# Kernel tuning notes

Hardware: AMD Instinct MI355X
Metric: run time of the kernel (lower is better)

The kernel has to match this reference:

```python
import jax, jax.numpy as jnp
import numpy as np

B, DIM, H, W = 8, 128, 128, 128
QK, MLP, HEADS, NT, GS = 128, 256, 4, 8, 128


def _ln(x, w, b):
    m = jnp.mean(x, -1, keepdims=True)
    v = jnp.mean((x - m) ** 2, -1, keepdims=True)
    return (x - m) * jax.lax.rsqrt(v + 1e-5) * w + b


def _norml2(x):
    n = jnp.sqrt(jnp.sum(x * x, -1, keepdims=True))
    return x / jnp.maximum(n, 1e-12)


def setup_inputs() -> dict:
    key = jax.random.key(0)
    ks = jax.random.split(key, 12)
    s = 0.02
    f32 = jnp.float32
    return {
        'x': jax.random.normal(ks[0], (B, DIM, H, W), f32),
        'means': jax.random.normal(ks[1], (NT, DIM), f32),
        'ln1_w': jnp.ones((DIM,), f32), 'ln1_b': jnp.zeros((DIM,), f32),
        'wq': jax.random.normal(ks[2], (QK, DIM), f32) * s,
        'wk': jax.random.normal(ks[3], (QK, DIM), f32) * s,
        'wv': jax.random.normal(ks[4], (DIM, DIM), f32) * s,
        'wproj': jax.random.normal(ks[5], (DIM, DIM), f32) * s,
        'irca_wk': jax.random.normal(ks[6], (QK, DIM), f32) * s,
        'irca_wv': jax.random.normal(ks[7], (DIM, DIM), f32) * s,
        'conv1x1_w': jax.random.normal(ks[8], (DIM, DIM), f32) * s,
        'ln2_w': jnp.ones((DIM,), f32), 'ln2_b': jnp.zeros((DIM,), f32),
        'fc1_w': jax.random.normal(ks[9], (MLP, DIM), f32) * s,
        'fc1_b': jnp.zeros((MLP,), f32),
        'dw_w': jax.random.normal(ks[10], (MLP, 1, 5, 5), f32) * s,
        'dw_b': jnp.zeros((MLP,), f32),
        'fc2_w': jax.random.normal(ks[11], (DIM, MLP), f32) * s,
        'fc2_b': jnp.zeros((DIM,), f32),
    }


def reference(x, means, ln1_w, ln1_b, wq, wk, wv, wproj, irca_wk, irca_wv,
              conv1x1_w, ln2_w, ln2_b, fc1_w, fc1_b, dw_w, dw_b, fc2_w, fc2_b):
    Bx, C, Hh, Ww = x.shape
    N = Hh * Ww
    xt = x.reshape(Bx, C, N).transpose(0, 2, 1)          # b n c
    residual = xt
    xn = _ln(xt, ln1_w, ln1_b)
    m = jax.lax.stop_gradient(means)                      # eval: means buffer, detached
    # IRCA (eval path): global K/V from cluster means
    dq, dv = QK // HEADS, C // HEADS
    kg = (m @ irca_wk.T).reshape(NT, HEADS, dq).transpose(1, 0, 2)  # h nt dq
    vg = (m @ irca_wv.T).reshape(NT, HEADS, dv).transpose(1, 0, 2)  # h nt dv
    # cluster assignment -> token reordering (no grad)
    scores = jnp.einsum('bic,jc->bij', _norml2(xn), _norml2(m))
    buckets = jnp.argmax(scores, axis=-1)
    idx = jnp.argsort(buckets, axis=-1)                   # [B,N] permutation
    # IASA
    q = xn @ wq.T
    k = xn @ wk.T
    v = xn @ wv.T
    take = lambda t: jnp.take_along_axis(t, idx[:, :, None], axis=1)
    q, k, v = take(q), take(k), take(v)
    gs = min(N, GS)
    ng = (N + gs - 1) // gs
    pad_n = ng * gs - N
    qp = jnp.concatenate([q, jnp.flip(q[:, N - pad_n:N], axis=1)], axis=1)
    qp = qp.reshape(Bx, ng, gs, HEADS, dq).transpose(0, 1, 3, 2, 4)  # b g h gs dq

    def window(t, d):
        tp = jnp.concatenate([t, jnp.flip(t[:, N - pad_n - gs:N], axis=1)], axis=1)
        blk = tp.reshape(Bx, ng + 1, gs, HEADS, d)
        win = jnp.concatenate([blk[:, :-1], blk[:, 1:]], axis=2)     # b g 2gs h d
        return win.transpose(0, 1, 3, 2, 4)

    kp = window(k, dq)
    vp = window(v, dv)
    scale = 1.0 / np.sqrt(dq)
    a1 = jax.nn.softmax(jnp.einsum('bghqd,bghkd->bghqk', qp, kp) * scale, axis=-1)
    out1 = jnp.einsum('bghqk,bghkd->bghqd', a1, vp)
    a2 = jax.nn.softmax(jnp.einsum('bghqd,hkd->bghqk', qp, kg) * scale, axis=-1)
    out2 = jnp.einsum('bghqk,hkd->bghqd', a2, vg)
    out = (out1 + out2).transpose(0, 1, 3, 2, 4).reshape(Bx, ng * gs, C)[:, :N]
    inv = jnp.argsort(idx, axis=-1)                       # scatter-back = inverse perm
    out = jnp.take_along_axis(out, inv[:, :, None], axis=1)
    out = out @ wproj.T
    yimg = out.transpose(0, 2, 1).reshape(Bx, C, Hh, Ww)
    yimg = jnp.einsum('oc,bchw->bohw', conv1x1_w, yimg)
    x2 = residual + yimg.reshape(Bx, C, N).transpose(0, 2, 1)
    # ConvFFN with PreNorm
    xm = _ln(x2, ln2_w, ln2_b)
    h1 = jax.nn.gelu(xm @ fc1_w.T + fc1_b, approximate=False)
    himg = h1.transpose(0, 2, 1).reshape(Bx, MLP, Hh, Ww)
    dwc = jax.lax.conv_general_dilated(himg, dw_w, (1, 1), 'SAME',
                                       feature_group_count=MLP,
                                       dimension_numbers=('NCHW', 'OIHW', 'NCHW'))
    dwc = jax.nn.gelu(dwc + dw_b.reshape(1, MLP, 1, 1), approximate=False)
    h1 = h1 + dwc.reshape(Bx, MLP, N).transpose(0, 2, 1)
    x3 = x2 + (h1 @ fc2_w.T + fc2_b)
    return x3.transpose(0, 2, 1).reshape(Bx, C, Hh, Ww)
```

## Files before the change

kernel.cpp:

```cpp
#include <hip/hip_runtime.h>
#include <math.h>

typedef unsigned short u16;
typedef unsigned int u32;
typedef __attribute__((ext_vector_type(8))) short bf16x8;
typedef __attribute__((ext_vector_type(4))) float f32x4;

constexpr int BB   = 8;
constexpr int DIMC = 128;
constexpr int HH   = 128;
constexpr int WW   = 128;
constexpr int NTOK = HH * WW;
constexpr int QKD  = 128;
constexpr int MLPD = 256;
constexpr int NTm  = 8;
constexpr int GSZ  = 128;
constexpr int NGRP = NTOK / GSZ;
constexpr size_t BIG = 16777216;

__device__ __forceinline__ float exp2_raw(float x) {
    return __builtin_amdgcn_exp2f(x);
}
__device__ __forceinline__ float gelu_f(float v) {
    float u = v * (0.7978845608028654f + 0.035677408136300125f * v * v);
    float e = exp2_raw(u * 2.885390081777927f);
    float th = 1.0f - 2.0f * __builtin_amdgcn_rcpf(e + 1.0f);
    return 0.5f * v * (1.0f + th);
}
__device__ __forceinline__ float b2f(u16 u) {
    return __uint_as_float(((u32)u) << 16);
}
__device__ __forceinline__ u16 f2b(float f) {
    u32 x = __float_as_uint(f);
    return (u16)((x + 0x7fffu + ((x >> 16) & 1u)) >> 16);
}
__device__ __forceinline__ float ulo(u32 u) { return __uint_as_float(u << 16); }
__device__ __forceinline__ float uhi(u32 u) { return __uint_as_float(u & 0xffff0000u); }

__global__ __launch_bounds__(128) void k_prep(const float* __restrict__ means,
        const float* __restrict__ iwk, const float* __restrict__ iwv,
        float* __restrict__ mhat, u16* __restrict__ kgbb, u16* __restrict__ vgtb) {
    __shared__ float sm[DIMC];
    __shared__ float inv_s;
    int tt = blockIdx.x;
    int t = threadIdx.x;
    sm[t] = means[tt * DIMC + t];
    __syncthreads();
    if (t == 0) {
        float s = 0.f;
        for (int c = 0; c < DIMC; c++) s += sm[c] * sm[c];
        inv_s = 1.f / fmaxf(sqrtf(s), 1e-12f);
    }
    __syncthreads();
    mhat[tt * DIMC + t] = sm[t] * inv_s;
    float sk = 0.f, sv = 0.f;
    #pragma unroll 8
    for (int c = 0; c < DIMC; c++) {
        sk = fmaf(sm[c], iwk[t * DIMC + c], sk);
        sv = fmaf(sm[c], iwv[t * DIMC + c], sv);
    }
    kgbb[tt * DIMC + t] = f2b(sk);
    vgtb[(t >> 5) * 256 + (t & 31) * 8 + tt] = f2b(sv);
}

__global__ __launch_bounds__(256) void k_cvtall(const float* __restrict__ wq,
        const float* __restrict__ wk, const float* __restrict__ wv,
        const float* __restrict__ fc1, const float* __restrict__ fc2,
        u16* __restrict__ wqkv, u16* __restrict__ fc1b, u16* __restrict__ fc2b) {
    int i = blockIdx.x * 256 + threadIdx.x;
    if (i < 49152) {
        const float* s = (i < 16384) ? wq : (i < 32768 ? wk : wv);
        wqkv[i] = f2b(s[i & 16383]);
    } else if (i < 81920) {
        fc1b[i - 49152] = f2b(fc1[i - 49152]);
    } else if (i < 114688) {
        fc2b[i - 81920] = f2b(fc2[i - 81920]);
    }
}

__global__ __launch_bounds__(256) void k_fuse(const float* __restrict__ c1,
        const float* __restrict__ wp, u16* __restrict__ wf) {
    __shared__ float wpS[DIMC * DIMC];
    int t = threadIdx.x;
    for (int i = t; i < DIMC * DIMC; i += 256) wpS[i] = wp[i];
    __syncthreads();
    int o = blockIdx.x * 2 + (t >> 7);
    int c = t & 127;
    float s = 0.f;
    #pragma unroll 8
    for (int m = 0; m < DIMC; m++) s = fmaf(c1[o * DIMC + m], wpS[m * DIMC + c], s);
    wf[o * DIMC + c] = f2b(s);
}

__global__ __launch_bounds__(256) void k_ln1(const float* __restrict__ x,
        const float* __restrict__ lw, const float* __restrict__ lb,
        const float* __restrict__ mhat, u16* __restrict__ xn, int* __restrict__ bucket) {
    __shared__ float smh[NTm * DIMC];
    __shared__ float lwb[DIMC], lbb[DIMC];
    __shared__ float red[4][64][3];
    __shared__ float scr[4][64][9];
    const int chunk = blockIdx.x;
    const int b = chunk >> 8;
    const int n0 = (chunk & 255) << 6;
    const int t = threadIdx.x;
    const int cg = t >> 6, tok = t & 63;
    const int n = n0 + tok;
    const int cbase = cg * 32;
    for (int i = t; i < NTm * DIMC; i += 256) smh[i] = mhat[i];
    if (t < DIMC) { lwb[t] = lw[t]; lbb[t] = lb[t]; }

    const float* xb = x + (size_t)b * DIMC * NTOK + (size_t)cbase * NTOK + n;
    float xv[32];
    float sum = 0.f, sq = 0.f;
    #pragma unroll
    for (int c = 0; c < 32; c++) {
        float v = xb[(size_t)c * NTOK];
        xv[c] = v;
        sum += v; sq += v * v;
    }
    red[cg][tok][0] = sum;
    red[cg][tok][1] = sq;
    __syncthreads();
    float s0 = red[0][tok][0] + red[1][tok][0] + red[2][tok][0] + red[3][tok][0];
    float q0 = red[0][tok][1] + red[1][tok][1] + red[2][tok][1] + red[3][tok][1];
    float mean = s0 * (1.0f / DIMC);
    float var = q0 * (1.0f / DIMC) - mean * mean;
    float rstd = rsqrtf(var + 1e-5f);

    float sc[NTm];
    #pragma unroll
    for (int j = 0; j < NTm; j++) sc[j] = 0.f;
    u32 opk[16];
    #pragma unroll
    for (int c = 0; c < 32; c += 2) {
        float v0 = (xv[c]     - mean) * rstd * lwb[cbase + c]     + lbb[cbase + c];
        float v1 = (xv[c + 1] - mean) * rstd * lwb[cbase + c + 1] + lbb[cbase + c + 1];
        #pragma unroll
        for (int j = 0; j < NTm; j++) {
            sc[j] = fmaf(v0, smh[j * DIMC + cbase + c], sc[j]);
            sc[j] = fmaf(v1, smh[j * DIMC + cbase + c + 1], sc[j]);
        }
        opk[c >> 1] = (u32)f2b(v0) | ((u32)f2b(v1) << 16);
    }
    u16* xnr = xn + ((size_t)b * NTOK + n) * DIMC + cbase;
    *(uint4*)(xnr + 0)  = make_uint4(opk[0],  opk[1],  opk[2],  opk[3]);
    *(uint4*)(xnr + 8)  = make_uint4(opk[4],  opk[5],  opk[6],  opk[7]);
    *(uint4*)(xnr + 16) = make_uint4(opk[8],  opk[9],  opk[10], opk[11]);
    *(uint4*)(xnr + 24) = make_uint4(opk[12], opk[13], opk[14], opk[15]);

    #pragma unroll
    for (int j = 0; j < NTm; j++) scr[cg][tok][j] = sc[j];
    __syncthreads();
    if (cg == 0) {
        float v0 = ((scr[0][tok][0] + scr[1][tok][0]) + (scr[2][tok][0] + scr[3][tok][0]));
        int best = 0; float bv = v0;
        #pragma unroll
        for (int j = 1; j < NTm; j++) {
            float v = ((scr[0][tok][j] + scr[1][tok][j]) + (scr[2][tok][j] + scr[3][tok][j]));
            if (v > bv) { bv = v; best = j; }
        }
        bucket[b * NTOK + n] = best;
    }
}

__global__ __launch_bounds__(64) void k_count(const int* __restrict__ bucket, int* __restrict__ cnt) {
    int chunk = blockIdx.x;
    int bk = bucket[(chunk << 6) + threadIdx.x];
    #pragma unroll
    for (int j = 0; j < NTm; j++) {
        unsigned long long m = __ballot(bk == j);
        if (threadIdx.x == 0) cnt[chunk * NTm + j] = (int)__popcll(m);
    }
}

__global__ __launch_bounds__(64) void k_scan(const int* __restrict__ cnt, int* __restrict__ base) {
    __shared__ int sc[256 * NTm];
    __shared__ int bb[NTm], tot[NTm];
    int b = blockIdx.x, t = threadIdx.x;
    for (int i = t; i < 256 * NTm; i += 64) sc[i] = cnt[b * 256 * NTm + i];
    __syncthreads();
    if (t < NTm) {
        int run = 0;
        for (int c = 0; c < 256; c++) {
            int v = sc[c * NTm + t];
            sc[c * NTm + t] = run;
            run += v;
        }
        tot[t] = run;
    }
    __syncthreads();
    if (t == 0) {
        int a = 0;
        for (int j = 0; j < NTm; j++) { bb[j] = a; a += tot[j]; }
    }
    __syncthreads();
    for (int i = t; i < 256 * NTm; i += 64) base[b * 256 * NTm + i] = sc[i] + bb[i & 7];
}

__global__ __launch_bounds__(64) void k_place(const int* __restrict__ bucket,
        const int* __restrict__ base, int* __restrict__ gidx) {
    int chunk = blockIdx.x;
    int lane = threadIdx.x;
    int nf = (chunk << 6) + lane;
    int bk = bucket[nf];
    unsigned long long lower = (1ull << lane) - 1ull;
    int rank = 0;
    #pragma unroll
    for (int j = 0; j < NTm; j++) {
        unsigned long long m = __ballot(bk == j);
        if (bk == j) rank = (int)__popcll(m & lower);
    }
    int b = nf >> 14;
    int pos = base[chunk * NTm + bk] + rank;
    gidx[b * NTOK + pos] = nf & (NTOK - 1);
}

__global__ __launch_bounds__(256) void k_inv(const int* __restrict__ gidx, u16* __restrict__ iinv) {
    int i = blockIdx.x * 256 + threadIdx.x;
    int b = i >> 14;
    iinv[((size_t)b << 14) + gidx[i]] = (u16)(i & (NTOK - 1));
}

template<int KDIM, int NOUT, int GATHER, int AIMG, int BIASF, int GELUF, int RES, int STIMG, int CBF, int LN2F>
__global__ __launch_bounds__(256) void g_mfma(const u16* __restrict__ A, const u16* __restrict__ W,
        const float* __restrict__ bias, const void* __restrict__ resid,
        const int* __restrict__ gidx, void* __restrict__ Cout, float ascale,
        const float* __restrict__ lnw, const float* __restrict__ lnb, void* __restrict__ Cout2) {
    __shared__ u16 As[128 * 40];
    __shared__ u16 Ws[128 * 40];
    const int b = blockIdx.z;
    const int m0 = blockIdx.x * 128;
    const int n0 = blockIdx.y * 128;
    const int t = threadIdx.x;
    const int lane = t & 63;
    const int wave = t >> 6;
    const int wm = (wave & 1) * 64;
    const int wn = (wave >> 1) * 64;
    const int srow = t >> 2;
    const int sko = (t & 3) * 8;
    const u16* pA0 = nullptr; const u16* pA1 = nullptr;
    if (!AIMG) {
        int ra0 = m0 + srow, ra1 = m0 + 64 + srow;
        if (GATHER == 1) {
            ra0 = gidx[b * NTOK + ra0];
            ra1 = gidx[b * NTOK + ra1];
        } else if (GATHER == 2) {
            const u16* gi = (const u16*)gidx;
            ra0 = gi[b * NTOK + ra0];
            ra1 = gi[b * NTOK + ra1];
        }
        pA0 = A + ((size_t)b * NTOK + ra0) * KDIM + sko;
        pA1 = A + ((size_t)b * NTOK + ra1) * KDIM + sko;
    }
    const u16* pW0 = W + (size_t)(n0 + srow) * KDIM + sko;
    const u16* pW1 = W + (size_t)(n0 + 64 + srow) * KDIM + sko;

    f32x4 acc[4][4];
    #pragma unroll
    for (int i = 0; i < 4; i++)
        #pragma unroll
        for (int j = 0; j < 4; j++) acc[i][j] = (f32x4){0.f, 0.f, 0.f, 0.f};

    for (int k0 = 0; k0 < KDIM; k0 += 32) {
        uint4 a0, a1, w0, w1;
        u16 e[16];
        if (!AIMG) {
            a0 = *(const uint4*)(pA0 + k0);
            a1 = *(const uint4*)(pA1 + k0);
        } else {
            const int kk2 = t & 31;
            const int tg = t >> 5;
            const u16* src = A + ((size_t)b * KDIM + k0 + kk2) * NTOK + m0 + tg * 16;
            *(uint4*)&e[0] = *(const uint4*)src;
            *(uint4*)&e[8] = *(const uint4*)(src + 8);
        }
        w0 = *(const uint4*)(pW0 + k0);
        w1 = *(const uint4*)(pW1 + k0);
        __syncthreads();
        if (!AIMG) {
            *(uint4*)&As[srow * 40 + sko] = a0;
            *(uint4*)&As[(64 + srow) * 40 + sko] = a1;
        } else {
            const int kk2 = t & 31;
            const int tg = t >> 5;
            #pragma unroll
            for (int j = 0; j < 16; j++) As[(tg * 16 + j) * 40 + kk2] = e[j];
        }
        *(uint4*)&Ws[srow * 40 + sko] = w0;
        *(uint4*)&Ws[(64 + srow) * 40 + sko] = w1;
        __syncthreads();
        bf16x8 af[4], bfv[4];
        #pragma unroll
        for (int i = 0; i < 4; i++)
            af[i] = *(bf16x8*)&As[(wm + i * 16 + (lane & 15)) * 40 + (lane >> 4) * 8];
        #pragma unroll
        for (int j = 0; j < 4; j++)
            bfv[j] = *(bf16x8*)&Ws[(wn + j * 16 + (lane & 15)) * 40 + (lane >> 4) * 8];
        #pragma unroll
        for (int i = 0; i < 4; i++)
            #pragma unroll
            for (int j = 0; j < 4; j++)
                acc[i][j] = __builtin_amdgcn_mfma_f32_16x16x32_bf16(af[i], bfv[j], acc[i][j], 0, 0, 0);
    }

    const int c2 = lane & 15, gq2 = lane >> 4;
    int colj[4];
    #pragma unroll
    for (int j = 0; j < 4; j++) colj[j] = n0 + wn + j * 16 + c2;

    if (LN2F) {
        #pragma unroll
        for (int i = 0; i < 4; i++) {
            int rbase = m0 + wm + i * 16 + gq2 * 4;
            #pragma unroll
            for (int j = 0; j < 4; j++) {
                const float* rf = (const float*)resid;
                float4 rr = *(const float4*)&rf[((size_t)b * NOUT + colj[j]) * NTOK + rbase];
                acc[i][j][0] += rr.x; acc[i][j][1] += rr.y;
                acc[i][j][2] += rr.z; acc[i][j][3] += rr.w;
            }
        }
        __syncthreads();
        float* ps = (float*)&As[0];
        const int h = wn >> 6;
        float mean_[4][4], rstd_[4][4];
        #pragma unroll
        for (int i = 0; i < 4; i++)
            #pragma unroll
            for (int r = 0; r < 4; r++) {
                float s = 0.f, q = 0.f;
                #pragma unroll
                for (int j = 0; j < 4; j++) { float tv = acc[i][j][r]; s += tv; q += tv * tv; }
                s += __shfl_xor(s, 1, 64); q += __shfl_xor(q, 1, 64);
                s += __shfl_xor(s, 2, 64); q += __shfl_xor(q, 2, 64);
                s += __shfl_xor(s, 4, 64); q += __shfl_xor(q, 4, 64);
                s += __shfl_xor(s, 8, 64); q += __shfl_xor(q, 8, 64);
                if (c2 == 0) {
                    int rl = wm + i * 16 + gq2 * 4 + r;
                    ps[(h * 128 + rl) * 2 + 0] = s;
                    ps[(h * 128 + rl) * 2 + 1] = q;
                }
            }
        __syncthreads();
        #pragma unroll
        for (int i = 0; i < 4; i++)
            #pragma unroll
            for (int r = 0; r < 4; r++) {
                int rl = wm + i * 16 + gq2 * 4 + r;
                float s = ps[rl * 2 + 0] + ps[(128 + rl) * 2 + 0];
                float q = ps[rl * 2 + 1] + ps[(128 + rl) * 2 + 1];
                float mn = s * (1.0f / 128.0f);
                float vr = q * (1.0f / 128.0f) - mn * mn;
                mean_[i][r] = mn;
                rstd_[i][r] = rsqrtf(vr + 1e-5f);
            }
        float lwj[4], lbj[4];
        #pragma unroll
        for (int j = 0; j < 4; j++) { lwj[j] = lnw[colj[j]]; lbj[j] = lnb[colj[j]]; }
        u16* xo = (u16*)Cout;
        u16* mo = (u16*)Cout2;
        #pragma unroll
        for (int i = 0; i < 4; i++) {
            int rbase = m0 + wm + i * 16 + gq2 * 4;
            #pragma unroll
            for (int j = 0; j < 4; j++)
                #pragma unroll
                for (int r = 0; r < 4; r++) {
                    float tv = acc[i][j][r];
                    size_t off = ((size_t)b * NTOK + rbase + r) * NOUT + colj[j];
                    xo[off] = f2b(tv);
                    mo[off] = f2b((tv - mean_[i][r]) * rstd_[i][r] * lwj[j] + lbj[j]);
                }
        }
        return;
    }

    const float smul = (blockIdx.y == 0) ? ascale : 1.0f;
    float bj[4];
    #pragma unroll
    for (int j = 0; j < 4; j++) bj[j] = BIASF ? bias[colj[j]] : 0.f;
    #pragma unroll
    for (int i = 0; i < 4; i++) {
        int rbase = m0 + wm + i * 16 + gq2 * 4;
        #pragma unroll
        for (int j = 0; j < 4; j++) {
            f32x4 v = acc[i][j];
            v[0] *= smul; v[1] *= smul; v[2] *= smul; v[3] *= smul;
            if (BIASF) { v[0] += bj[j]; v[1] += bj[j]; v[2] += bj[j]; v[3] += bj[j]; }
            if (GELUF) { v[0] = gelu_f(v[0]); v[1] = gelu_f(v[1]); v[2] = gelu_f(v[2]); v[3] = gelu_f(v[3]); }
            if (RES == 1) {
                const float* rf = (const float*)resid;
                float4 rr = *(const float4*)&rf[((size_t)b * NOUT + colj[j]) * NTOK + rbase];
                v[0] += rr.x; v[1] += rr.y; v[2] += rr.z; v[3] += rr.w;
            } else if (RES == 3) {
                const u16* rb = (const u16*)resid;
                #pragma unroll
                for (int r = 0; r < 4; r++)
                    v[r] += b2f(rb[((size_t)b * NTOK + rbase + r) * NOUT + colj[j]]);
            }
            if (STIMG) {
                size_t off = ((size_t)b * NOUT + colj[j]) * NTOK + rbase;
                if (CBF) {
                    ushort4 o;
                    o.x = f2b(v[0]); o.y = f2b(v[1]); o.z = f2b(v[2]); o.w = f2b(v[3]);
                    *(ushort4*)((u16*)Cout + off) = o;
                } else {
                    *(float4*)((float*)Cout + off) = make_float4(v[0], v[1], v[2], v[3]);
                }
            } else {
                if (CBF) {
                    #pragma unroll
                    for (int r = 0; r < 4; r++)
                        ((u16*)Cout)[((size_t)b * NTOK + rbase + r) * NOUT + colj[j]] = f2b(v[r]);
                } else {
                    #pragma unroll
                    for (int r = 0; r < 4; r++)
                        ((float*)Cout)[((size_t)b * NTOK + rbase + r) * NOUT + colj[j]] = v[r];
                }
            }
        }
    }
}

__global__ __launch_bounds__(256, 3) void k_attn(const u16* __restrict__ qkv,
        const u16* __restrict__ kgbb, const u16* __restrict__ vgtb,
        u16* __restrict__ outp) {
    __shared__ u16 VT[2][32][264];
    __shared__ u16 Pb[4][64][36];
    const int g = blockIdx.x, hp = blockIdx.y, b = blockIdx.z;
    const int t = threadIdx.x;
    const int wave = t >> 6, lane = t & 63;
    const int c = lane & 15, gq = lane >> 4;
    const int lh = wave & 1, head = hp * 2 + lh, qh = wave >> 1;
    const size_t brow = (size_t)b * NTOK;
    const bool lastg = (g == NGRP - 1);

    {
        int key = t;
        int pos = (!lastg || key < GSZ) ? g * GSZ + key : NTOK - 1 - (key - GSZ);
        const u16* vp = qkv + (brow + pos) * 384 + 256 + hp * 64;
        #pragma unroll
        for (int i = 0; i < 8; i++) {
            uint4 v = *(const uint4*)(vp + i * 8);
            u16 e[8];
            *(uint4*)e = v;
            #pragma unroll
            for (int j = 0; j < 8; j++) {
                int d = i * 8 + j;
                VT[d >> 5][d & 31][key] = e[j];
            }
        }
        if (t < 64) {
            int l2 = t >> 5, dv = t & 31;
            uint4 v = *(const uint4*)(vgtb + ((size_t)(hp * 2 + l2) * 32 + dv) * 8);
            *(uint4*)&VT[l2][dv][256] = v;
        }
    }

    const int q0 = g * GSZ + qh * 64;
    bf16x8 qf[4];
    #pragma unroll
    for (int nq = 0; nq < 4; nq++)
        qf[nq] = *(const bf16x8*)(qkv + (brow + q0 + nq * 16 + c) * 384 + head * 32 + gq * 8);

    const u16* kbp = qkv + brow * 384 + 128 + head * 32 + gq * 8;
    bf16x8 kfa[8][2];
    #pragma unroll
    for (int s = 0; s < 8; s++)
        #pragma unroll
        for (int mk = 0; mk < 2; mk++) {
            int kl = s * 32 + mk * 16 + c;
            int pos = (!lastg || kl < GSZ) ? g * GSZ + kl : NTOK - 1 - (kl - GSZ);
            kfa[s][mk] = *(const bf16x8*)(kbp + (size_t)pos * 384);
        }
    bf16x8 kgf = *(const bf16x8*)(kgbb + (c & 7) * 128 + head * 32 + gq * 8);

    __syncthreads();

    f32x4 acc[4][2];
    #pragma unroll
    for (int i = 0; i < 4; i++)
        #pragma unroll
        for (int j = 0; j < 2; j++) acc[i][j] = (f32x4){0.f, 0.f, 0.f, 0.f};
    float lsum[4] = {0.f, 0.f, 0.f, 0.f};

    __builtin_amdgcn_s_setprio(1);
    for (int s = 0; s < 8; s++) {
        #pragma unroll
        for (int mk = 0; mk < 2; mk++) {
            #pragma unroll
            for (int nq = 0; nq < 4; nq++) {
                f32x4 st = __builtin_amdgcn_mfma_f32_16x16x32_bf16(kfa[s][mk], qf[nq],
                        (f32x4){0.f, 0.f, 0.f, 0.f}, 0, 0, 0);
                float p0 = exp2_raw(st[0]), p1 = exp2_raw(st[1]);
                float p2 = exp2_raw(st[2]), p3 = exp2_raw(st[3]);
                lsum[nq] += (p0 + p1) + (p2 + p3);
                u32 r0, r1;
                asm("v_cvt_pk_bf16_f32 %0, %1, %2" : "=v"(r0) : "v"(p0), "v"(p1));
                asm("v_cvt_pk_bf16_f32 %0, %1, %2" : "=v"(r1) : "v"(p2), "v"(p3));
                *(uint2*)&Pb[wave][nq * 16 + c][mk * 16 + gq * 4] = make_uint2(r0, r1);
            }
        }
        __builtin_amdgcn_sched_barrier(0);
        bf16x8 pf[4], vf[2];
        #pragma unroll
        for (int mt = 0; mt < 4; mt++)
            pf[mt] = *(const bf16x8*)&Pb[wave][mt * 16 + c][gq * 8];
        #pragma unroll
        for (int nv = 0; nv < 2; nv++)
            vf[nv] = *(const bf16x8*)&VT[lh][nv * 16 + c][s * 32 + gq * 8];
        #pragma unroll
        for (int mt = 0; mt < 4; mt++)
            #pragma unroll
            for (int nv = 0; nv < 2; nv++)
                acc[mt][nv] = __builtin_amdgcn_mfma_f32_16x16x32_bf16(pf[mt], vf[nv], acc[mt][nv], 0, 0, 0);
    }

    #pragma unroll
    for (int nq = 0; nq < 4; nq++) {
        lsum[nq] += __shfl_xor(lsum[nq], 16, 64);
        lsum[nq] += __shfl_xor(lsum[nq], 32, 64);
    }

    {
        #pragma unroll
        for (int nq = 0; nq < 4; nq++) {
            f32x4 sg = __builtin_amdgcn_mfma_f32_16x16x32_bf16(kgf, qf[nq],
                    (f32x4){0.f, 0.f, 0.f, 0.f}, 0, 0, 0);
            float p0, p1, p2, p3;
            if (gq < 2) {
                p0 = exp2_raw(sg[0]); p1 = exp2_raw(sg[1]);
                p2 = exp2_raw(sg[2]); p3 = exp2_raw(sg[3]);
            } else { p0 = p1 = p2 = p3 = 0.f; }
            float lg = (p0 + p1) + (p2 + p3);
            lg += __shfl_xor(lg, 16, 64);
            lg += __shfl_xor(lg, 32, 64);
            float w = lsum[nq] / lg;
            p0 *= w; p1 *= w; p2 *= w; p3 *= w;
            u32 r0, r1;
            asm("v_cvt_pk_bf16_f32 %0, %1, %2" : "=v"(r0) : "v"(p0), "v"(p1));
            asm("v_cvt_pk_bf16_f32 %0, %1, %2" : "=v"(r1) : "v"(p2), "v"(p3));
            *(uint2*)&Pb[wave][nq * 16 + c][gq * 4] = make_uint2(r0, r1);
        }
        __builtin_amdgcn_sched_barrier(0);
        bf16x8 zf;
        #pragma unroll
        for (int z8 = 0; z8 < 8; z8++) zf[z8] = 0;
        bf16x8 pf[4], vf[2];
        #pragma unroll
        for (int mt = 0; mt < 4; mt++)
            pf[mt] = *(const bf16x8*)&Pb[wave][mt * 16 + c][gq * 8];
        #pragma unroll
        for (int nv = 0; nv < 2; nv++)
            vf[nv] = (gq == 0) ? *(const bf16x8*)&VT[lh][nv * 16 + c][256] : zf;
        #pragma unroll
        for (int mt = 0; mt < 4; mt++)
            #pragma unroll
            for (int nv = 0; nv < 2; nv++)
                acc[mt][nv] = __builtin_amdgcn_mfma_f32_16x16x32_bf16(pf[mt], vf[nv], acc[mt][nv], 0, 0, 0);
    }
    __builtin_amdgcn_s_setprio(0);

    float* lf = (float*)&Pb[wave][0][0];
    if (gq == 0) {
        #pragma unroll
        for (int nq = 0; nq < 4; nq++) lf[nq * 16 + c] = lsum[nq];
    }
    __builtin_amdgcn_sched_barrier(0);
    u16 ov[4][2][4];
    #pragma unroll
    for (int mt = 0; mt < 4; mt++) {
        float il[4];
        #pragma unroll
        for (int r = 0; r < 4; r++)
            il[r] = 1.f / lf[mt * 16 + gq * 4 + r];
        #pragma unroll
        for (int nv = 0; nv < 2; nv++)
            #pragma unroll
            for (int r = 0; r < 4; r++)
                ov[mt][nv][r] = f2b(acc[mt][nv][r] * il[r]);
    }

    __syncthreads();
    u16* st = (u16*)&VT[0][0][0];
    #pragma unroll
    for (int mt = 0; mt < 4; mt++)
        #pragma unroll
        for (int nv = 0; nv < 2; nv++)
            #pragma unroll
            for (int r = 0; r < 4; r++)
                st[(qh * 64 + mt * 16 + gq * 4 + r) * 68 + lh * 32 + nv * 16 + c] = ov[mt][nv][r];
    __syncthreads();
    {
        const int rl0 = t >> 3;
        const int seg = t & 7;
        #pragma unroll
        for (int p = 0; p < 4; p++) {
            int rl = rl0 + p * 32;
            uint4 v4 = *(const uint4*)&st[rl * 68 + seg * 8];
            *(uint4*)&outp[(brow + g * GSZ + rl) * 128 + hp * 64 + seg * 8] = v4;
        }
    }
}

__global__ __launch_bounds__(256) void k_dw(const u16* __restrict__ himg,
        const float* __restrict__ dww, const float* __restrict__ dwb, u16* __restrict__ dsum) {
    const int mc = blockIdx.y, b = blockIdx.z;
    const int t = threadIdx.x;
    const int y = blockIdx.x * 32 + (t >> 4) * 2;
    const int xb = (t & 15) * 8;
    float wgt[25];
    #pragma unroll
    for (int i = 0; i < 25; i++) wgt[i] = dww[mc * 25 + i];
    const float bsv = dwb[mc];
    const u16* src = himg + ((size_t)b * MLPD + mc) * NTOK;
    u16* dst = dsum + ((size_t)b * MLPD + mc) * NTOK;

    float w[6][12];
    #pragma unroll
    for (int r = 0; r < 6; r++) {
        int ysrc = y - 2 + r;
        bool vy = (ysrc >= 0 && ysrc < HH);
        const u16* rp = src + ysrc * WW + xb;
        uint4 aq = vy ? *(const uint4*)(rp - 8) : make_uint4(0u, 0u, 0u, 0u);
        uint4 bq = vy ? *(const uint4*)(rp)     : make_uint4(0u, 0u, 0u, 0u);
        uint4 cq = vy ? *(const uint4*)(rp + 8) : make_uint4(0u, 0u, 0u, 0u);
        w[r][0]  = ulo(aq.w); w[r][1]  = uhi(aq.w);
        w[r][2]  = ulo(bq.x); w[r][3]  = uhi(bq.x);
        w[r][4]  = ulo(bq.y); w[r][5]  = uhi(bq.y);
        w[r][6]  = ulo(bq.z); w[r][7]  = uhi(bq.z);
        w[r][8]  = ulo(bq.w); w[r][9]  = uhi(bq.w);
        w[r][10] = ulo(cq.x); w[r][11] = uhi(cq.x);
        if (xb == 0)   { w[r][0]  = 0.f; w[r][1]  = 0.f; }
        if (xb == 120) { w[r][10] = 0.f; w[r][11] = 0.f; }
    }

    float acc0[8], acc1[8];
    #pragma unroll
    for (int px = 0; px < 8; px++) { acc0[px] = 0.f; acc1[px] = 0.f; }
    #pragma unroll
    for (int dy = 0; dy < 5; dy++)
        #pragma unroll
        for (int dx = 0; dx < 5; dx++) {
            float wv = wgt[dy * 5 + dx];
            #pragma unroll
            for (int px = 0; px < 8; px++) {
                acc0[px] = fmaf(wv, w[dy][px + dx], acc0[px]);
                acc1[px] = fmaf(wv, w[dy + 1][px + dx], acc1[px]);
            }
        }

    u32 o0[4], o1[4];
    #pragma unroll
    for (int px = 0; px < 8; px += 2) {
        u16 a0 = f2b(w[2][px + 2] + gelu_f(acc0[px] + bsv));
        u16 a1 = f2b(w[2][px + 3] + gelu_f(acc0[px + 1] + bsv));
        o0[px >> 1] = (u32)a0 | ((u32)a1 << 16);
        u16 b0 = f2b(w[3][px + 2] + gelu_f(acc1[px] + bsv));
        u16 b1 = f2b(w[3][px + 3] + gelu_f(acc1[px + 1] + bsv));
        o1[px >> 1] = (u32)b0 | ((u32)b1 << 16);
    }
    *(uint4*)(dst + y * WW + xb) = *(uint4*)o0;
    *(uint4*)(dst + (y + 1) * WW + xb) = *(uint4*)o1;
}

extern "C" void kernel_launch(void* const* d_in, const int* in_sizes, int n_in,
                              void* d_out, int out_size, void* d_ws, size_t ws_size,
                              hipStream_t stream) {
    const float* x       = (const float*)d_in[0];
    const float* means   = (const float*)d_in[1];
    const float* ln1_w   = (const float*)d_in[2];
    const float* ln1_b   = (const float*)d_in[3];
    const float* wq      = (const float*)d_in[4];
    const float* wk      = (const float*)d_in[5];
    const float* wv      = (const float*)d_in[6];
    const float* wproj   = (const float*)d_in[7];
    const float* irca_wk = (const float*)d_in[8];
    const float* irca_wv = (const float*)d_in[9];
    const float* conv1w  = (const float*)d_in[10];
    const float* ln2_w   = (const float*)d_in[11];
    const float* ln2_b   = (const float*)d_in[12];
    const float* fc1_w   = (const float*)d_in[13];
    const float* fc1_b   = (const float*)d_in[14];
    const float* dw_w    = (const float*)d_in[15];
    const float* dw_b    = (const float*)d_in[16];
    const float* fc2_w   = (const float*)d_in[17];
    const float* fc2_b   = (const float*)d_in[18];
    float* out = (float*)d_out;

    const size_t need = 202514432;
    if (ws_size < need) return;

    char* base = (char*)d_ws;
    float* mhat  = (float*)(base);
    u16*   kgbb  = (u16*)(base + 4096);
    u16*   vgtb  = (u16*)(base + 6144);
    int*   bucket = (int*)(base + 8192);
    u16*   wqkv  = (u16*)(base + 8192);
    u16*   wfub  = wqkv + 3 * 16384;
    u16*   fc1b  = wfub + 16384;
    u16*   fc2b  = fc1b + 32768;
    u16*   iinv  = (u16*)(base + 270336);
    int*   cnt   = (int*)(base + 532480);
    int*   cbase = (int*)(base + 598016);
    int*   gidx  = (int*)(base + 663552);
    u16*   Abase = (u16*)(base + 1187840);
    u16*   x2b   = (u16*)(base + 101851136);
    u16*   dsum  = (u16*)(base + 135405568);

    u16* qkv  = Abase;
    u16* himg = Abase;
    u16* xmb  = Abase + 2 * BIG;
    u16* xnb   = (u16*)d_out;
    u16* attnb = (u16*)d_out;

    k_prep<<<NTm, 128, 0, stream>>>(means, irca_wk, irca_wv, mhat, kgbb, vgtb);
    k_ln1<<<BB * NTOK / 64, 256, 0, stream>>>(x, ln1_w, ln1_b, mhat, xnb, bucket);
    k_count<<<BB * NTOK / 64, 64, 0, stream>>>(bucket, cnt);
    k_scan<<<BB, 64, 0, stream>>>(cnt, cbase);
    k_place<<<BB * NTOK / 64, 64, 0, stream>>>(bucket, cbase, gidx);
    k_inv<<<BB * NTOK / 256, 256, 0, stream>>>(gidx, iinv);

    k_cvtall<<<448, 256, 0, stream>>>(wq, wk, wv, fc1_w, fc2_w, wqkv, fc1b, fc2b);
    k_fuse<<<64, 256, 0, stream>>>(conv1w, wproj, wfub);

    const float qsc2 = 0.25503489924160945f;
    g_mfma<128, 384, 1, 0, 0, 0, 0, 0, 1, 0><<<dim3(128, 3, BB), 256, 0, stream>>>(
        xnb, wqkv, nullptr, nullptr, gidx, qkv, qsc2, nullptr, nullptr, nullptr);

    k_attn<<<dim3(NGRP, 2, BB), 256, 0, stream>>>(qkv, kgbb, vgtb, attnb);

    g_mfma<128, 128, 2, 0, 0, 0, 1, 0, 1, 1><<<dim3(128, 1, BB), 256, 0, stream>>>(
        attnb, wfub, nullptr, x, (const int*)iinv, x2b, 1.0f, ln2_w, ln2_b, xmb);

    g_mfma<128, 256, 0, 0, 1, 1, 0, 1, 1, 0><<<dim3(128, 2, BB), 256, 0, stream>>>(
        xmb, fc1b, fc1_b, nullptr, nullptr, himg, 1.0f, nullptr, nullptr, nullptr);
    k_dw<<<dim3(4, MLPD, BB), 256, 0, stream>>>(himg, dw_w, dw_b, dsum);
    g_mfma<256, 128, 0, 1, 1, 0, 3, 1, 0, 0><<<dim3(128, 1, BB), 256, 0, stream>>>(
        dsum, fc2b, fc2_b, x2b, nullptr, out, 1.0f, nullptr, nullptr, nullptr);

    (void)in_sizes; (void)n_in; (void)out_size;
}
```

Baseline: 291.7 us.

## Halve attention V shared buffer and stage second key half via registers

The V-transpose shared buffer in the attention kernel shrinks to half the keys. The second half of V and the global V values are prefetched into registers and written to LDS after the first half has been consumed, with block barriers around the swap. Launch bounds rise from 3 to 4 blocks per SM to exploit the smaller LDS footprint, and the s_setprio hints are removed. This trades extra barriers and register pressure (holding vh1 and vg) for higher occupancy, and it risks spilling under the tighter register cap.

```diff
diff --git a/kernel.cpp b/kernel.cpp
--- a/kernel.cpp
+++ b/kernel.cpp
@@ -422,10 +422,10 @@
     }
 }
 
-__global__ __launch_bounds__(256, 3) void k_attn(const u16* __restrict__ qkv,
+__global__ __launch_bounds__(256, 4) void k_attn(const u16* __restrict__ qkv,
         const u16* __restrict__ kgbb, const u16* __restrict__ vgtb,
         u16* __restrict__ outp) {
-    __shared__ u16 VT[2][32][264];
+    __shared__ u16 VT[2][32][136];
     __shared__ u16 Pb[4][64][36];
     const int g = blockIdx.x, hp = blockIdx.y, b = blockIdx.z;
     const int t = threadIdx.x;
@@ -436,25 +436,35 @@
     const bool lastg = (g == NGRP - 1);
 
     {
-        int key = t;
-        int pos = (!lastg || key < GSZ) ? g * GSZ + key : NTOK - 1 - (key - GSZ);
-        const u16* vp = qkv + (brow + pos) * 384 + 256 + hp * 64;
-        #pragma unroll
-        for (int i = 0; i < 8; i++) {
+        const int key = t >> 1;
+        const int ch0 = (t & 1) * 32;
+        const u16* vp = qkv + (brow + g * GSZ + key) * 384 + 256 + hp * 64 + ch0;
+        #pragma unroll
+        for (int i = 0; i < 4; i++) {
             uint4 v = *(const uint4*)(vp + i * 8);
             u16 e[8];
             *(uint4*)e = v;
             #pragma unroll
             for (int j = 0; j < 8; j++) {
-                int d = i * 8 + j;
+                int d = ch0 + i * 8 + j;
                 VT[d >> 5][d & 31][key] = e[j];
             }
         }
-        if (t < 64) {
-            int l2 = t >> 5, dv = t & 31;
-            uint4 v = *(const uint4*)(vgtb + ((size_t)(hp * 2 + l2) * 32 + dv) * 8);
-            *(uint4*)&VT[l2][dv][256] = v;
-        }
+    }
+
+    uint4 vh1[4];
+    {
+        const int key = 128 + (t >> 1);
+        const int ch0 = (t & 1) * 32;
+        int pos = (!lastg) ? g * GSZ + key : NTOK - 1 - (key - GSZ);
+        const u16* vp = qkv + (brow + pos) * 384 + 256 + hp * 64 + ch0;
+        #pragma unroll
+        for (int i = 0; i < 4; i++) vh1[i] = *(const uint4*)(vp + i * 8);
+    }
+    uint4 vg;
+    if (t < 64) {
+        int l2 = t >> 5, dv = t & 31;
+        vg = *(const uint4*)(vgtb + ((size_t)(hp * 2 + l2) * 32 + dv) * 8);
     }
 
     const int q0 = g * GSZ + qh * 64;
@@ -484,36 +494,62 @@
         for (int j = 0; j < 2; j++) acc[i][j] = (f32x4){0.f, 0.f, 0.f, 0.f};
     float lsum[4] = {0.f, 0.f, 0.f, 0.f};
 
-    __builtin_amdgcn_s_setprio(1);
-    for (int s = 0; s < 8; s++) {
-        #pragma unroll
-        for (int mk = 0; mk < 2; mk++) {
-            #pragma unroll
-            for (int nq = 0; nq < 4; nq++) {
-                f32x4 st = __builtin_amdgcn_mfma_f32_16x16x32_bf16(kfa[s][mk], qf[nq],
-                        (f32x4){0.f, 0.f, 0.f, 0.f}, 0, 0, 0);
-                float p0 = exp2_raw(st[0]), p1 = exp2_raw(st[1]);
-                float p2 = exp2_raw(st[2]), p3 = exp2_raw(st[3]);
-                lsum[nq] += (p0 + p1) + (p2 + p3);
-                u32 r0, r1;
-                asm("v_cvt_pk_bf16_f32 %0, %1, %2" : "=v"(r0) : "v"(p0), "v"(p1));
-                asm("v_cvt_pk_bf16_f32 %0, %1, %2" : "=v"(r1) : "v"(p2), "v"(p3));
-                *(uint2*)&Pb[wave][nq * 16 + c][mk * 16 + gq * 4] = make_uint2(r0, r1);
-            }
-        }
-        __builtin_amdgcn_sched_barrier(0);
-        bf16x8 pf[4], vf[2];
-        #pragma unroll
-        for (int mt = 0; mt < 4; mt++)
-            pf[mt] = *(const bf16x8*)&Pb[wave][mt * 16 + c][gq * 8];
-        #pragma unroll
-        for (int nv = 0; nv < 2; nv++)
-            vf[nv] = *(const bf16x8*)&VT[lh][nv * 16 + c][s * 32 + gq * 8];
-        #pragma unroll
-        for (int mt = 0; mt < 4; mt++)
+    #pragma unroll
+    for (int half = 0; half < 2; half++) {
+        if (half == 1) {
+            __syncthreads();
+            {
+                const int key = t >> 1;
+                const int ch0 = (t & 1) * 32;
+                #pragma unroll
+                for (int i = 0; i < 4; i++) {
+                    u16 e[8];
+                    *(uint4*)e = vh1[i];
+                    #pragma unroll
+                    for (int j = 0; j < 8; j++) {
+                        int d = ch0 + i * 8 + j;
+                        VT[d >> 5][d & 31][key] = e[j];
+                    }
+                }
+                if (t < 64) {
+                    int l2 = t >> 5, dv = t & 31;
+                    *(uint4*)&VT[l2][dv][128] = vg;
+                }
+            }
+            __syncthreads();
+        }
+        #pragma unroll
+        for (int s2 = 0; s2 < 4; s2++) {
+            const int s = half * 4 + s2;
+            #pragma unroll
+            for (int mk = 0; mk < 2; mk++) {
+                #pragma unroll
+                for (int nq = 0; nq < 4; nq++) {
+                    f32x4 st = __builtin_amdgcn_mfma_f32_16x16x32_bf16(kfa[s][mk], qf[nq],
+                            (f32x4){0.f, 0.f, 0.f, 0.f}, 0, 0, 0);
+                    float p0 = exp2_raw(st[0]), p1 = exp2_raw(st[1]);
+                    float p2 = exp2_raw(st[2]), p3 = exp2_raw(st[3]);
+                    lsum[nq] += (p0 + p1) + (p2 + p3);
+                    u32 r0, r1;
+                    asm("v_cvt_pk_bf16_f32 %0, %1, %2" : "=v"(r0) : "v"(p0), "v"(p1));
+                    asm("v_cvt_pk_bf16_f32 %0, %1, %2" : "=v"(r1) : "v"(p2), "v"(p3));
+                    *(uint2*)&Pb[wave][nq * 16 + c][mk * 16 + gq * 4] = make_uint2(r0, r1);
+                }
+            }
+            __builtin_amdgcn_sched_barrier(0);
+            bf16x8 pf[4], vf[2];
+            #pragma unroll
+            for (int mt = 0; mt < 4; mt++)
+                pf[mt] = *(const bf16x8*)&Pb[wave][mt * 16 + c][gq * 8];
             #pragma unroll
             for (int nv = 0; nv < 2; nv++)
-                acc[mt][nv] = __builtin_amdgcn_mfma_f32_16x16x32_bf16(pf[mt], vf[nv], acc[mt][nv], 0, 0, 0);
+                vf[nv] = *(const bf16x8*)&VT[lh][nv * 16 + c][s2 * 32 + gq * 8];
+            #pragma unroll
+            for (int mt = 0; mt < 4; mt++)
+                #pragma unroll
+                for (int nv = 0; nv < 2; nv++)
+                    acc[mt][nv] = __builtin_amdgcn_mfma_f32_16x16x32_bf16(pf[mt], vf[nv], acc[mt][nv], 0, 0, 0);
+        }
     }
 
     #pragma unroll
@@ -552,14 +588,13 @@
             pf[mt] = *(const bf16x8*)&Pb[wave][mt * 16 + c][gq * 8];
         #pragma unroll
         for (int nv = 0; nv < 2; nv++)
-            vf[nv] = (gq == 0) ? *(const bf16x8*)&VT[lh][nv * 16 + c][256] : zf;
+            vf[nv] = (gq == 0) ? *(const bf16x8*)&VT[lh][nv * 16 + c][128] : zf;
         #pragma unroll
         for (int mt = 0; mt < 4; mt++)
             #pragma unroll
             for (int nv = 0; nv < 2; nv++)
                 acc[mt][nv] = __builtin_amdgcn_mfma_f32_16x16x32_bf16(pf[mt], vf[nv], acc[mt][nv], 0, 0, 0);
     }
-    __builtin_amdgcn_s_setprio(0);
 
     float* lf = (float*)&Pb[wave][0][0];
     if (gq == 0) {
```

After: 395.9 us. +35.7%, slower.
